# Kernel tuning notes

Hardware: AMD Instinct MI355X
Metric: run time of the kernel (lower is better)

Reference implementation:

```python
import jax, jax.numpy as jnp
import numpy as np

GC = 128      # mem_dim
HEADS = 4     # gc / att_head_dim
HD = 32       # att_head_dim


def _dwconv(x, w, b, pad):
    # depthwise conv, NCHW, weight OIHW with I=1, groups=GC
    y = jax.lax.conv_general_dilated(
        x, w, window_strides=(1, 1),
        padding=((pad[0], pad[0]), (pad[1], pad[1])),
        feature_group_count=GC,
        dimension_numbers=('NCHW', 'OIHW', 'NCHW'))
    return y + b[None, :, None, None]


def setup_inputs() -> dict:
    key = jax.random.key(0)
    ks = jax.random.split(key, 5)
    x = jax.random.normal(ks[0], (32, 512, 56, 56), dtype=jnp.float32)
    w_dw1 = jax.random.normal(ks[1], (GC, 1, 3, 3), dtype=jnp.float32) * 0.1
    b_dw1 = jnp.zeros((GC,), jnp.float32)
    w_dw2 = jax.random.normal(ks[2], (GC, 1, 7, 7), dtype=jnp.float32) * 0.05
    b_dw2 = jnp.zeros((GC,), jnp.float32)
    w_qk = jax.random.normal(ks[3], (2 * GC, GC, 1, 1), dtype=jnp.float32) * (1.0 / np.sqrt(GC))
    b_qk = jnp.zeros((2 * GC,), jnp.float32)
    return {"x": x, "w_dw1": w_dw1, "b_dw1": b_dw1, "w_dw2": w_dw2,
            "b_dw2": b_dw2, "w_qk": w_qk, "b_qk": b_qk}


def reference(x, w_dw1, b_dw1, w_dw2, b_dw2, w_qk, b_qk):
    B, C, H, W = x.shape
    HW = H * W
    # grasp_memory + asymmetric_decouple (split along channels)
    m0 = C - 3 * GC
    mem = x[:, :m0]
    feat_att = x[:, m0:m0 + GC]
    feat_conv1 = x[:, m0 + GC:m0 + 2 * GC]
    feat_conv2 = x[:, m0 + 2 * GC:]
    feat_conv1 = _dwconv(feat_conv1, w_dw1, b_dw1, (1, 1))
    feat_conv2 = _dwconv(feat_conv2, w_dw2, b_dw2, (3, 3))
    # 1x1 conv qk -> [B, 2*GC, H, W]
    qk = jnp.einsum('bchw,oc->bohw', feat_att, w_qk[:, :, 0, 0]) + b_qk[None, :, None, None]
    qk = qk.reshape(B, 2 * GC, HW)
    q = qk[:, :GC].reshape(B, HEADS, HD, HW).transpose(0, 1, 3, 2)   # [B,h,HW,d]
    k = qk[:, GC:].reshape(B, HEADS, HD, HW).transpose(0, 1, 3, 2)
    v = feat_att.reshape(B, HEADS, HD, HW).transpose(0, 1, 3, 2)
    q = jax.nn.elu(q) + 1.0
    k = jax.nn.elu(k) + 1.0
    kmean = k.mean(axis=2, keepdims=True)                            # [B,h,1,d]
    z = 1.0 / (jnp.einsum('bhnd,bhmd->bhnm', q, kmean) + 1e-6)       # [B,h,HW,1]
    kv = jnp.einsum('bhnd,bhne->bhde', k, v) / HW                    # [B,h,d,d]
    att = jnp.einsum('bhnd,bhde->bhne', q, kv) * z                   # [B,h,HW,d]
    feat_att_out = att.transpose(0, 1, 3, 2).reshape(B, GC, H, W)
    feats = jnp.concatenate([feat_att_out, feat_conv1, feat_conv2], axis=1)
    return (mem, feats)
```

## Files before the change

kernel.cpp:

```cpp
#include <hip/hip_runtime.h>
#include <hip/hip_bf16.h>

#define Bn   32
#define Cn   512
#define GCn  128
#define HWn  3136
#define M0   128

#define Q_ELEMS  (Bn*GCn*HWn)
#define KV_ELEMS (Bn*4*32*32)
#define KS_ELEMS (Bn*4*32)

typedef __attribute__((ext_vector_type(8))) short bf16x8;
typedef __attribute__((ext_vector_type(4))) float f32x4;

__device__ __forceinline__ float bf2f(unsigned short u) {
    union { unsigned int i; float f; } v; v.i = ((unsigned int)u) << 16; return v.f;
}
__device__ __forceinline__ unsigned short f2bf(float f) {
    union { __hip_bfloat16 h; unsigned short u; } v; v.h = __float2bfloat16(f); return v.u;
}
__device__ __forceinline__ float act_elu1(float v) {
    return v > 0.0f ? v + 1.0f : __expf(v);
}

__global__ void k_wt(const float* __restrict__ w_qk, unsigned short* __restrict__ wfrag) {
    int idx = blockIdx.x * 256 + threadIdx.x;
    int j  = idx & 7;
    int l  = (idx >> 3) & 63;
    int ks = (idx >> 9) & 3;
    int mt = idx >> 11;
    int o = mt * 16 + (l & 15);
    int c = ks * 32 + (l >> 4) * 8 + j;
    wfrag[idx] = f2bf(w_qk[o * 128 + c]);
}

__global__ void k_copy(const float* __restrict__ x, float* __restrict__ out) {
    long long idx4 = (long long)blockIdx.x * 256 + threadIdx.x;
    int b = (int)(idx4 / 100352);
    int r = (int)(idx4 % 100352);
    ((float4*)out)[idx4] = ((const float4*)x)[(long long)b * 401408 + r];
}

__global__ __launch_bounds__(256) void k_qkgemm(
    const float* __restrict__ x, const unsigned short* __restrict__ wfrag,
    const float* __restrict__ b_qk,
    unsigned short* __restrict__ q_ws, unsigned short* __restrict__ k_ws) {

    __shared__ float Xl[128 * 66];

    const int t  = threadIdx.x;
    const int n0 = blockIdx.x * 64;
    const int b  = blockIdx.y;
    const float* xa = x + ((long long)(b * Cn + M0)) * HWn;

    #pragma unroll
    for (int p = 0; p < 8; ++p) {
        int idx4 = p * 256 + t;
        int c = idx4 >> 4, j4 = idx4 & 15;
        float4 v = *(const float4*)(xa + (long long)c * HWn + n0 + j4 * 4);
        float* d = Xl + c * 66 + j4 * 4;
        *(float2*)(d)     = make_float2(v.x, v.y);
        *(float2*)(d + 2) = make_float2(v.z, v.w);
    }
    __syncthreads();

    const int w = t >> 6, l = t & 63, nn = l & 15, q = l >> 4;
    f32x4 acc[4][4] = {};

    #pragma unroll
    for (int ks = 0; ks < 4; ++ks) {
        bf16x8 bq[4];
        #pragma unroll
        for (int in = 0; in < 4; ++in) {
            const float* src = Xl + (ks * 32 + q * 8) * 66 + in * 16 + nn;
            short tmp[8];
            #pragma unroll
            for (int j = 0; j < 8; ++j) tmp[j] = (short)f2bf(src[j * 66]);
            bq[in] = *(bf16x8*)tmp;
        }
        #pragma unroll
        for (int im = 0; im < 4; ++im) {
            const int mt = 4 * w + im;
            bf16x8 aq = *(const bf16x8*)(wfrag + ((mt * 4 + ks) * 64 + l) * 8);
            #pragma unroll
            for (int in = 0; in < 4; ++in)
                acc[im][in] = __builtin_amdgcn_mfma_f32_16x16x32_bf16(aq, bq[in], acc[im][in], 0, 0, 0);
        }
    }

    #pragma unroll
    for (int im = 0; im < 4; ++im) {
        const int obase = w * 64 + im * 16 + q * 4;
        float4 bias4 = *(const float4*)(b_qk + obase);
        unsigned short* dst_ws = (w < 2) ? q_ws : k_ws;
        const int orow = obase & 127;
        #pragma unroll
        for (int r = 0; r < 4; ++r) {
            const float bias = ((const float*)&bias4)[r];
            unsigned short* dst = dst_ws + ((long long)(b * GCn + orow + r)) * HWn + n0 + nn;
            #pragma unroll
            for (int in = 0; in < 4; ++in)
                dst[in * 16] = f2bf(act_elu1(acc[im][in][r] + bias));
        }
    }
}

__global__ __launch_bounds__(256) void k_kv(
    const float* __restrict__ x, const unsigned short* __restrict__ k_ws,
    float* __restrict__ kv_g, float* __restrict__ ks_g) {

    const int t = threadIdx.x, w = t >> 6, l = t & 63, nn = l & 15, q = l >> 4;
    const int g = blockIdx.x, h = blockIdx.y, b = blockIdx.z;
    const int dm = w >> 1, en = w & 1;
    const int d = h * 32 + dm * 16 + nn;
    const int e = h * 32 + en * 16 + nn;
    const unsigned short* kp = k_ws + ((long long)(b * GCn + d)) * HWn;
    const float* vp = x + ((long long)(b * Cn + M0 + e)) * HWn;

    f32x4 acc = {};
    float ksl = 0.f;
    for (int ks = 0; ks < 14; ++ks) {
        const int n = g * 448 + ks * 32 + q * 8;
        bf16x8 aq = *(const bf16x8*)(kp + n);
        float4 v0 = *(const float4*)(vp + n);
        float4 v1 = *(const float4*)(vp + n + 4);
        short tb[8];
        tb[0] = (short)f2bf(v0.x); tb[1] = (short)f2bf(v0.y);
        tb[2] = (short)f2bf(v0.z); tb[3] = (short)f2bf(v0.w);
        tb[4] = (short)f2bf(v1.x); tb[5] = (short)f2bf(v1.y);
        tb[6] = (short)f2bf(v1.z); tb[7] = (short)f2bf(v1.w);
        bf16x8 bq = *(bf16x8*)tb;
        acc = __builtin_amdgcn_mfma_f32_16x16x32_bf16(aq, bq, acc, 0, 0, 0);
        if (en == 0) {
            const unsigned short* au = (const unsigned short*)&aq;
            #pragma unroll
            for (int j = 0; j < 8; ++j) ksl += bf2f(au[j]);
        }
    }
    const int bh = b * 4 + h;
    #pragma unroll
    for (int r = 0; r < 4; ++r)
        atomicAdd(&kv_g[(bh << 10) + (dm * 16 + q * 4 + r) * 32 + en * 16 + nn], acc[r]);
    if (en == 0) atomicAdd(&ks_g[bh * 32 + dm * 16 + nn], ksl);
}

__global__ __launch_bounds__(256) void k_att(
    const unsigned short* __restrict__ q_ws, const float* __restrict__ kv_g,
    const float* __restrict__ ks_g, float* __restrict__ feats) {

    __shared__ float kvl[1024];
    __shared__ float kml[32];
    const int t = threadIdx.x, h = blockIdx.y, b = blockIdx.z;
    const int bh = b * 4 + h;
    const float inv = 1.0f / 3136.0f;
    #pragma unroll
    for (int p = 0; p < 4; ++p) kvl[t + p * 256] = kv_g[(bh << 10) + t + p * 256] * inv;
    if (t < 32) kml[t] = ks_g[bh * 32 + t] * inv;
    __syncthreads();

    const int n2 = blockIdx.x * 256 + t;
    if (n2 >= 1568) return;
    const unsigned short* qp = q_ws + ((long long)(b * GCn + h * 32)) * HWn + n2 * 2;
    float a0[32], a1[32];
    float z0 = 1e-6f, z1 = 1e-6f;
    #pragma unroll
    for (int e = 0; e < 32; ++e) { a0[e] = 0.f; a1[e] = 0.f; }
    #pragma unroll 4
    for (int d = 0; d < 32; ++d) {
        const unsigned int qq = *(const unsigned int*)(qp + (long long)d * HWn);
        const float q0 = bf2f((unsigned short)qq);
        const float q1 = bf2f((unsigned short)(qq >> 16));
        z0 = __builtin_fmaf(q0, kml[d], z0);
        z1 = __builtin_fmaf(q1, kml[d], z1);
        #pragma unroll
        for (int e = 0; e < 32; ++e) {
            const float kv = kvl[d * 32 + e];
            a0[e] = __builtin_fmaf(q0, kv, a0[e]);
            a1[e] = __builtin_fmaf(q1, kv, a1[e]);
        }
    }
    z0 = 1.f / z0; z1 = 1.f / z1;
    float* op = feats + ((long long)(b * 384 + h * 32)) * HWn + n2 * 2;
    #pragma unroll
    for (int e = 0; e < 32; ++e)
        *(float2*)(op + (long long)e * HWn) = make_float2(a0[e] * z0, a1[e] * z1);
}

template<int KS, int PAD, int CIN, int COUT>
__global__ __launch_bounds__(256) void k_dwconv(
    const float* __restrict__ x, const float* __restrict__ wg,
    const float* __restrict__ bg, float* __restrict__ feats) {

    const int c = blockIdx.x, b = blockIdx.y;
    const float* in = x + ((long long)(b * Cn + CIN + c)) * HWn;
    float* op = feats + ((long long)(b * 384 + COUT + c)) * HWn;

    float wr[KS * KS];
    #pragma unroll
    for (int i = 0; i < KS * KS; ++i) wr[i] = wg[c * KS * KS + i];
    const float bias = bg[c];

    for (int item = threadIdx.x; item < 784; item += 256) {
        const int y  = item / 14;
        const int xq = (item % 14) * 4;
        float acc[4] = {bias, bias, bias, bias};
        #pragma unroll
        for (int dy = 0; dy < KS; ++dy) {
            const int yy = y + dy - PAD;
            if (yy < 0 || yy >= 56) continue;
            const float* row = in + yy * 56 + xq;
            float r[12];
            float4 f;
            if (xq >= 4) f = *(const float4*)(row - 4); else f = make_float4(0, 0, 0, 0);
            r[0] = f.x; r[1] = f.y; r[2] = f.z; r[3] = f.w;
            f = *(const float4*)(row);
            r[4] = f.x; r[5] = f.y; r[6] = f.z; r[7] = f.w;
            if (xq <= 48) f = *(const float4*)(row + 4); else f = make_float4(0, 0, 0, 0);
            r[8] = f.x; r[9] = f.y; r[10] = f.z; r[11] = f.w;
            #pragma unroll
            for (int dx = 0; dx < KS; ++dx) {
                const float wv = wr[dy * KS + dx];
                #pragma unroll
                for (int j = 0; j < 4; ++j)
                    acc[j] = __builtin_fmaf(wv, r[j + dx + 4 - PAD], acc[j]);
            }
        }
        *(float4*)(op + y * 56 + xq) = make_float4(acc[0], acc[1], acc[2], acc[3]);
    }
}

extern "C" void kernel_launch(void* const* d_in, const int* in_sizes, int n_in,
                              void* d_out, int out_size, void* d_ws, size_t ws_size,
                              hipStream_t stream) {
    const float* x     = (const float*)d_in[0];
    const float* w_dw1 = (const float*)d_in[1];
    const float* b_dw1 = (const float*)d_in[2];
    const float* w_dw2 = (const float*)d_in[3];
    const float* b_dw2 = (const float*)d_in[4];
    const float* w_qk  = (const float*)d_in[5];
    const float* b_qk  = (const float*)d_in[6];
    float* out = (float*)d_out;

    unsigned short* q_ws = (unsigned short*)d_ws;
    unsigned short* k_ws = q_ws + (long long)Q_ELEMS;
    float* kv_g = (float*)(k_ws + (long long)Q_ELEMS);
    float* ks_g = kv_g + KV_ELEMS;
    unsigned short* wfrag = (unsigned short*)(ks_g + KS_ELEMS);

    float* mem_out = out;
    float* feats   = out + (long long)Bn * GCn * HWn;

    hipMemsetAsync(kv_g, 0, (KV_ELEMS + KS_ELEMS) * sizeof(float), stream);
    k_wt  <<<128, 256, 0, stream>>>(w_qk, wfrag);
    k_copy<<<12544, 256, 0, stream>>>(x, mem_out);
    k_qkgemm<<<dim3(49, 32), 256, 0, stream>>>(x, wfrag, b_qk, q_ws, k_ws);
    k_kv  <<<dim3(7, 4, 32), 256, 0, stream>>>(x, k_ws, kv_g, ks_g);
    k_att <<<dim3(7, 4, 32), 256, 0, stream>>>(q_ws, kv_g, ks_g, feats);
    k_dwconv<3, 1, 256, 128><<<dim3(128, 32), 256, 0, stream>>>(x, w_dw1, b_dw1, feats);
    k_dwconv<7, 3, 384, 256><<<dim3(128, 32), 256, 0, stream>>>(x, w_dw2, b_dw2, feats);
}
```

Baseline: 494.1 us.

## Fuse KV reduction into QK GEMM and merge post kernels into one launch

Computes the K·V outer-product reduction and K column sums directly from shared memory inside the QK GEMM kernel. The K projection is no longer written to global workspace and then re-read along with V. The weight conversion and the kv zeroing are merged into one pre kernel. Attention, both depthwise convolutions and the mem copy now run as one heterogeneous-block launch, cutting launches and letting independent work overlap, at the cost of more LDS in the GEMM kernel and more atomics (one set per 64-column tile).

```diff
diff --git a/kernel.cpp b/kernel.cpp
--- a/kernel.cpp
+++ b/kernel.cpp
@@ -24,30 +24,33 @@
     return v > 0.0f ? v + 1.0f : __expf(v);
 }
 
-__global__ void k_wt(const float* __restrict__ w_qk, unsigned short* __restrict__ wfrag) {
-    int idx = blockIdx.x * 256 + threadIdx.x;
-    int j  = idx & 7;
-    int l  = (idx >> 3) & 63;
-    int ks = (idx >> 9) & 3;
-    int mt = idx >> 11;
-    int o = mt * 16 + (l & 15);
-    int c = ks * 32 + (l >> 4) * 8 + j;
-    wfrag[idx] = f2bf(w_qk[o * 128 + c]);
-}
-
-__global__ void k_copy(const float* __restrict__ x, float* __restrict__ out) {
-    long long idx4 = (long long)blockIdx.x * 256 + threadIdx.x;
-    int b = (int)(idx4 / 100352);
-    int r = (int)(idx4 % 100352);
-    ((float4*)out)[idx4] = ((const float4*)x)[(long long)b * 401408 + r];
-}
-
-__global__ __launch_bounds__(256) void k_qkgemm(
+__global__ __launch_bounds__(256) void k_pre(
+    const float* __restrict__ w_qk, unsigned short* __restrict__ wfrag,
+    float* __restrict__ kvz) {
+    const int t = threadIdx.x;
+    if (blockIdx.x < 128) {
+        int idx = blockIdx.x * 256 + t;
+        int j  = idx & 7;
+        int l  = (idx >> 3) & 63;
+        int ks = (idx >> 9) & 3;
+        int mt = idx >> 11;
+        int o = mt * 16 + (l & 15);
+        int c = ks * 32 + (l >> 4) * 8 + j;
+        wfrag[idx] = f2bf(w_qk[o * 128 + c]);
+    } else {
+        int i = (blockIdx.x - 128) * 256 + t;
+        kvz[i] = 0.0f;
+    }
+}
+
+__global__ __launch_bounds__(256) void k_main(
     const float* __restrict__ x, const unsigned short* __restrict__ wfrag,
     const float* __restrict__ b_qk,
-    unsigned short* __restrict__ q_ws, unsigned short* __restrict__ k_ws) {
+    unsigned short* __restrict__ q_ws, float* __restrict__ kv_g,
+    float* __restrict__ ks_g) {
 
     __shared__ float Xl[128 * 66];
+    __shared__ unsigned short Klds[128 * 72];
 
     const int t  = threadIdx.x;
     const int n0 = blockIdx.x * 64;
@@ -93,65 +96,75 @@
     for (int im = 0; im < 4; ++im) {
         const int obase = w * 64 + im * 16 + q * 4;
         float4 bias4 = *(const float4*)(b_qk + obase);
-        unsigned short* dst_ws = (w < 2) ? q_ws : k_ws;
-        const int orow = obase & 127;
-        #pragma unroll
-        for (int r = 0; r < 4; ++r) {
-            const float bias = ((const float*)&bias4)[r];
-            unsigned short* dst = dst_ws + ((long long)(b * GCn + orow + r)) * HWn + n0 + nn;
-            #pragma unroll
-            for (int in = 0; in < 4; ++in)
-                dst[in * 16] = f2bf(act_elu1(acc[im][in][r] + bias));
-        }
-    }
-}
-
-__global__ __launch_bounds__(256) void k_kv(
-    const float* __restrict__ x, const unsigned short* __restrict__ k_ws,
-    float* __restrict__ kv_g, float* __restrict__ ks_g) {
-
-    const int t = threadIdx.x, w = t >> 6, l = t & 63, nn = l & 15, q = l >> 4;
-    const int g = blockIdx.x, h = blockIdx.y, b = blockIdx.z;
-    const int dm = w >> 1, en = w & 1;
-    const int d = h * 32 + dm * 16 + nn;
-    const int e = h * 32 + en * 16 + nn;
-    const unsigned short* kp = k_ws + ((long long)(b * GCn + d)) * HWn;
-    const float* vp = x + ((long long)(b * Cn + M0 + e)) * HWn;
-
-    f32x4 acc = {};
-    float ksl = 0.f;
-    for (int ks = 0; ks < 14; ++ks) {
-        const int n = g * 448 + ks * 32 + q * 8;
-        bf16x8 aq = *(const bf16x8*)(kp + n);
-        float4 v0 = *(const float4*)(vp + n);
-        float4 v1 = *(const float4*)(vp + n + 4);
-        short tb[8];
-        tb[0] = (short)f2bf(v0.x); tb[1] = (short)f2bf(v0.y);
-        tb[2] = (short)f2bf(v0.z); tb[3] = (short)f2bf(v0.w);
-        tb[4] = (short)f2bf(v1.x); tb[5] = (short)f2bf(v1.y);
-        tb[6] = (short)f2bf(v1.z); tb[7] = (short)f2bf(v1.w);
-        bf16x8 bq = *(bf16x8*)tb;
-        acc = __builtin_amdgcn_mfma_f32_16x16x32_bf16(aq, bq, acc, 0, 0, 0);
-        if (en == 0) {
-            const unsigned short* au = (const unsigned short*)&aq;
-            #pragma unroll
-            for (int j = 0; j < 8; ++j) ksl += bf2f(au[j]);
+        if (w < 2) {
+            #pragma unroll
+            for (int r = 0; r < 4; ++r) {
+                const float bias = ((const float*)&bias4)[r];
+                unsigned short* dst = q_ws + ((long long)(b * GCn + obase + r)) * HWn + n0 + nn;
+                #pragma unroll
+                for (int in = 0; in < 4; ++in)
+                    dst[in * 16] = f2bf(act_elu1(acc[im][in][r] + bias));
+            }
+        } else {
+            const int krow = obase - 128;
+            #pragma unroll
+            for (int r = 0; r < 4; ++r) {
+                const float bias = ((const float*)&bias4)[r];
+                #pragma unroll
+                for (int in = 0; in < 4; ++in)
+                    Klds[(krow + r) * 72 + in * 16 + nn] = f2bf(act_elu1(acc[im][in][r] + bias));
+            }
+        }
+    }
+    __syncthreads();
+
+    const int h = w;
+    f32x4 akv[2][2] = {};
+    float ksl0 = 0.0f, ksl1 = 0.0f;
+    #pragma unroll
+    for (int kt = 0; kt < 2; ++kt) {
+        bf16x8 af0 = *(const bf16x8*)(Klds + (h * 32 + nn) * 72 + kt * 32 + q * 8);
+        bf16x8 af1 = *(const bf16x8*)(Klds + (h * 32 + 16 + nn) * 72 + kt * 32 + q * 8);
+        {
+            const unsigned short* a0 = (const unsigned short*)&af0;
+            const unsigned short* a1 = (const unsigned short*)&af1;
+            #pragma unroll
+            for (int j = 0; j < 8; ++j) { ksl0 += bf2f(a0[j]); ksl1 += bf2f(a1[j]); }
+        }
+        #pragma unroll
+        for (int nt = 0; nt < 2; ++nt) {
+            const float* vsrc = Xl + (h * 32 + nt * 16 + nn) * 66 + kt * 32 + q * 8;
+            short tb[8];
+            #pragma unroll
+            for (int j = 0; j < 8; ++j) tb[j] = (short)f2bf(vsrc[j]);
+            bf16x8 bv = *(bf16x8*)tb;
+            akv[0][nt] = __builtin_amdgcn_mfma_f32_16x16x32_bf16(af0, bv, akv[0][nt], 0, 0, 0);
+            akv[1][nt] = __builtin_amdgcn_mfma_f32_16x16x32_bf16(af1, bv, akv[1][nt], 0, 0, 0);
         }
     }
     const int bh = b * 4 + h;
     #pragma unroll
-    for (int r = 0; r < 4; ++r)
-        atomicAdd(&kv_g[(bh << 10) + (dm * 16 + q * 4 + r) * 32 + en * 16 + nn], acc[r]);
-    if (en == 0) atomicAdd(&ks_g[bh * 32 + dm * 16 + nn], ksl);
-}
-
-__global__ __launch_bounds__(256) void k_att(
+    for (int mt = 0; mt < 2; ++mt)
+        #pragma unroll
+        for (int nt = 0; nt < 2; ++nt)
+            #pragma unroll
+            for (int r = 0; r < 4; ++r)
+                atomicAdd(&kv_g[(bh << 10) + (mt * 16 + q * 4 + r) * 32 + nt * 16 + nn],
+                          akv[mt][nt][r]);
+    float s0 = ksl0; s0 += __shfl_xor(s0, 16, 64); s0 += __shfl_xor(s0, 32, 64);
+    float s1 = ksl1; s1 += __shfl_xor(s1, 16, 64); s1 += __shfl_xor(s1, 32, 64);
+    if (l < 16) {
+        atomicAdd(&ks_g[bh * 32 + nn],      s0);
+        atomicAdd(&ks_g[bh * 32 + 16 + nn], s1);
+    }
+}
+
+__device__ __forceinline__ void att_dev(
     const unsigned short* __restrict__ q_ws, const float* __restrict__ kv_g,
-    const float* __restrict__ ks_g, float* __restrict__ feats) {
-
-    __shared__ float kvl[1024];
-    __shared__ float kml[32];
-    const int t = threadIdx.x, h = blockIdx.y, b = blockIdx.z;
+    const float* __restrict__ ks_g, float* __restrict__ feats,
+    float* kvl, float* kml, int gx, int h, int b) {
+
+    const int t = threadIdx.x;
     const int bh = b * 4 + h;
     const float inv = 1.0f / 3136.0f;
     #pragma unroll
@@ -159,7 +172,7 @@
     if (t < 32) kml[t] = ks_g[bh * 32 + t] * inv;
     __syncthreads();
 
-    const int n2 = blockIdx.x * 256 + t;
+    const int n2 = gx * 256 + t;
     if (n2 >= 1568) return;
     const unsigned short* qp = q_ws + ((long long)(b * GCn + h * 32)) * HWn + n2 * 2;
     float a0[32], a1[32];
@@ -188,11 +201,10 @@
 }
 
 template<int KS, int PAD, int CIN, int COUT>
-__global__ __launch_bounds__(256) void k_dwconv(
+__device__ __forceinline__ void dwconv_dev(
     const float* __restrict__ x, const float* __restrict__ wg,
-    const float* __restrict__ bg, float* __restrict__ feats) {
-
-    const int c = blockIdx.x, b = blockIdx.y;
+    const float* __restrict__ bg, float* __restrict__ feats, int c, int b) {
+
     const float* in = x + ((long long)(b * Cn + CIN + c)) * HWn;
     float* op = feats + ((long long)(b * 384 + COUT + c)) * HWn;
 
@@ -230,6 +242,37 @@
     }
 }
 
+__global__ __launch_bounds__(256) void k_post(
+    const float* __restrict__ x,
+    const unsigned short* __restrict__ q_ws, const float* __restrict__ kv_g,
+    const float* __restrict__ ks_g,
+    const float* __restrict__ w_dw1, const float* __restrict__ b_dw1,
+    const float* __restrict__ w_dw2, const float* __restrict__ b_dw2,
+    float* __restrict__ mem_out, float* __restrict__ feats) {
+
+    __shared__ float kvl[1024];
+    __shared__ float kml[32];
+    const int bid = blockIdx.x;
+
+    if (bid < 4096) {
+        dwconv_dev<7, 3, 384, 256>(x, w_dw2, b_dw2, feats, bid & 127, bid >> 7);
+    } else if (bid < 8192) {
+        const int r = bid - 4096;
+        dwconv_dev<3, 1, 256, 128>(x, w_dw1, b_dw1, feats, r & 127, r >> 7);
+    } else if (bid < 9088) {
+        const int r = bid - 8192;
+        const int b = r / 28, rem = r % 28;
+        att_dev(q_ws, kv_g, ks_g, feats, kvl, kml, rem % 7, rem / 7, b);
+    } else {
+        const int r = bid - 9088;
+        for (int i4 = r * 256 + (int)threadIdx.x; i4 < 3211264; i4 += 2048 * 256) {
+            int b  = i4 / 100352;
+            int rr = i4 - b * 100352;
+            ((float4*)mem_out)[i4] = ((const float4*)x)[(long long)b * 401408 + rr];
+        }
+    }
+}
+
 extern "C" void kernel_launch(void* const* d_in, const int* in_sizes, int n_in,
                               void* d_out, int out_size, void* d_ws, size_t ws_size,
                               hipStream_t stream) {
@@ -243,20 +286,15 @@
     float* out = (float*)d_out;
 
     unsigned short* q_ws = (unsigned short*)d_ws;
-    unsigned short* k_ws = q_ws + (long long)Q_ELEMS;
-    float* kv_g = (float*)(k_ws + (long long)Q_ELEMS);
+    float* kv_g = (float*)(q_ws + (long long)Q_ELEMS);
     float* ks_g = kv_g + KV_ELEMS;
     unsigned short* wfrag = (unsigned short*)(ks_g + KS_ELEMS);
 
     float* mem_out = out;
     float* feats   = out + (long long)Bn * GCn * HWn;
 
-    hipMemsetAsync(kv_g, 0, (KV_ELEMS + KS_ELEMS) * sizeof(float), stream);
-    k_wt  <<<128, 256, 0, stream>>>(w_qk, wfrag);
-    k_copy<<<12544, 256, 0, stream>>>(x, mem_out);
-    k_qkgemm<<<dim3(49, 32), 256, 0, stream>>>(x, wfrag, b_qk, q_ws, k_ws);
-    k_kv  <<<dim3(7, 4, 32), 256, 0, stream>>>(x, k_ws, kv_g, ks_g);
-    k_att <<<dim3(7, 4, 32), 256, 0, stream>>>(q_ws, kv_g, ks_g, feats);
-    k_dwconv<3, 1, 256, 128><<<dim3(128, 32), 256, 0, stream>>>(x, w_dw1, b_dw1, feats);
-    k_dwconv<7, 3, 384, 256><<<dim3(128, 32), 256, 0, stream>>>(x, w_dw2, b_dw2, feats);
-}
+    k_pre <<<656, 256, 0, stream>>>(w_qk, wfrag, kv_g);
+    k_main<<<dim3(49, 32), 256, 0, stream>>>(x, wfrag, b_qk, q_ws, kv_g, ks_g);
+    k_post<<<11136, 256, 0, stream>>>(x, q_ws, kv_g, ks_g,
+                                      w_dw1, b_dw1, w_dw2, b_dw2, mem_out, feats);
+}
```

Result: no change. 489.0 us (-1.0%).
